# Optimization experiments

Hardware: AMD Instinct MI355X
Metric: run time of the kernel (lower is better)

The kernel has to match this reference:

```python
import jax, jax.numpy as jnp
import numpy as np
from jax import lax

C = 128
HEADS = 8
WS = 8
HIDDEN = C * 4


def _ln2d(x, w, b, eps=1e-6):
    # channel-first LayerNorm over dim 1 of [B,C,H,W]
    u = x.mean(axis=1, keepdims=True)
    s = ((x - u) ** 2).mean(axis=1, keepdims=True)
    xh = (x - u) / jnp.sqrt(s + eps)
    return w[None, :, None, None] * xh + b[None, :, None, None]


def _partition(x, ws):
    # [B,C,H,W] -> [B*nW, ws*ws, C]
    B, C_, H, W = x.shape
    x = x.transpose(0, 2, 3, 1)  # BHWC
    x = x.reshape(B, H // ws, ws, W // ws, ws, C_)
    x = x.transpose(0, 1, 3, 2, 4, 5)
    return x.reshape(-1, ws * ws, C_)


def _reverse(x, ws, H, W, B):
    # [B*nW, ws*ws, C] -> [B,C,H,W]
    C_ = x.shape[-1]
    x = x.reshape(B, H // ws, W // ws, ws, ws, C_)
    x = x.transpose(0, 1, 3, 2, 4, 5).reshape(B, H, W, C_)
    return x.transpose(0, 3, 1, 2)


def setup_inputs() -> dict:
    key = jax.random.key(0)
    ks = jax.random.split(key, 16)
    B, H, W = 4, 256, 256
    inp = {
        "x": jax.random.normal(ks[0], (B, C, H, W), jnp.float32),
        "l0": jax.random.uniform(ks[1], (B, 1, H, W), jnp.float32),
        "norm1_w": jnp.ones((C,), jnp.float32),
        "norm1_b": jnp.zeros((C,), jnp.float32),
        "norm2_w": jnp.ones((C,), jnp.float32),
        "norm2_b": jnp.zeros((C,), jnp.float32),
        "qkv_w": jax.random.normal(ks[2], (3 * C, C), jnp.float32) * (1.0 / np.sqrt(C)),
        "gate_w": jax.random.normal(ks[3], (C,), jnp.float32),
        "gate_b": jnp.zeros((C,), jnp.float32),
        "proj_w": jax.random.normal(ks[4], (C, C), jnp.float32) * (1.0 / np.sqrt(C)),
        "proj_b": jnp.zeros((C,), jnp.float32),
        "ffn_w1": jax.random.normal(ks[5], (HIDDEN, C), jnp.float32) * (1.0 / np.sqrt(C)),
        "ffn_b1": jnp.zeros((HIDDEN,), jnp.float32),
        "ffn_dw": jax.random.normal(ks[6], (HIDDEN, 1, 3, 3), jnp.float32) * (1.0 / 3.0),
        "ffn_dwb": jnp.zeros((HIDDEN,), jnp.float32),
        "ffn_w2": jax.random.normal(ks[7], (C, HIDDEN), jnp.float32) * (1.0 / np.sqrt(HIDDEN)),
        "ffn_b2": jnp.zeros((C,), jnp.float32),
    }
    return inp


def reference(x, l0, norm1_w, norm1_b, norm2_w, norm2_b, qkv_w, gate_w, gate_b,
              proj_w, proj_b, ffn_w1, ffn_b1, ffn_dw, ffn_dwb, ffn_w2, ffn_b2):
    B, C_, H, W = x.shape
    ws = WS
    # H,W chosen divisible by ws -> no padding branch
    head_dim = C_ // HEADS
    scale = head_dim ** -0.5

    shortcut = x
    xn = _ln2d(x, norm1_w, norm1_b)
    qkv = jnp.einsum("oc,bchw->bohw", qkv_w, xn)
    q, k, v = jnp.split(qkv, 3, axis=1)

    # illumination gate (l0 already at [H,W]; bilinear resize to same size is identity)
    gate = jax.nn.sigmoid(l0 * gate_w[None, :, None, None] + gate_b[None, :, None, None])
    q = q * gate

    q = _partition(q, ws)  # [Bw, ws*ws, C]
    k = _partition(k, ws)
    v = _partition(v, ws)
    Bw, N, _ = q.shape
    q = q.reshape(Bw, N, HEADS, head_dim)
    k = k.reshape(Bw, N, HEADS, head_dim)
    v = v.reshape(Bw, N, HEADS, head_dim)

    attn = jnp.einsum("bqhd,bkhd->bhqk", q, k) * scale
    attn = jax.nn.softmax(attn, axis=-1)
    out = jnp.einsum("bhqk,bkhd->bqhd", attn, v).reshape(Bw, N, C_)
    out = _reverse(out, ws, H, W, B)

    out = jnp.einsum("oc,bchw->bohw", proj_w, out) + proj_b[None, :, None, None]
    out = out + shortcut

    # FFN: 1x1 -> GELU -> depthwise 3x3 -> GELU -> 1x1
    h = _ln2d(out, norm2_w, norm2_b)
    h = jnp.einsum("oc,bchw->bohw", ffn_w1, h) + ffn_b1[None, :, None, None]
    h = jax.nn.gelu(h, approximate=False)
    h = lax.conv_general_dilated(h, ffn_dw, window_strides=(1, 1), padding="SAME",
                                 dimension_numbers=("NCHW", "OIHW", "NCHW"),
                                 feature_group_count=HIDDEN)
    h = h + ffn_dwb[None, :, None, None]
    h = jax.nn.gelu(h, approximate=False)
    h = jnp.einsum("oc,bchw->bohw", ffn_w2, h) + ffn_b2[None, :, None, None]
    return out + h
```

## Files before the change

### kernel.cpp

```cpp
#include <hip/hip_runtime.h>
#include <hip/hip_bf16.h>

#define HW   65536
#define CHW  (128*65536)
#define QKV_OZ  33554432u
#define QKV_H   1048576u
#define QKV_WIN 1024u

typedef __attribute__((ext_vector_type(8))) short bf16x8;
typedef __attribute__((ext_vector_type(4))) short bf16x4;
typedef __attribute__((ext_vector_type(4))) float f32x4;

__device__ __forceinline__ float geluf(float v){
    float u = 0.7978845608028654f * v * (1.f + 0.044715f*v*v);
    float e = __expf(2.f*u);
    float th = 1.f - 2.f/(e+1.f);
    return 0.5f*v*(1.f+th);
}

__device__ __forceinline__ float sigmoidf_(float z){
    return 1.f / (1.f + __expf(-z));
}

__device__ __forceinline__ float bf2f(short s){
    return __uint_as_float(((unsigned)(unsigned short)s) << 16);
}

__global__ __launch_bounds__(256) void k_cvt(
    const float* __restrict__ src, __hip_bfloat16* __restrict__ dst, int n)
{
    int i = blockIdx.x*256 + threadIdx.x;
    if (i < n) dst[i] = __float2bfloat16(src[i]);
}

__global__ __launch_bounds__(512,2) void k_ln_qkv_mfma(
    const float* __restrict__ x, const float* __restrict__ l0,
    const float* __restrict__ n1w, const float* __restrict__ n1b,
    const __hip_bfloat16* __restrict__ qkvw, const float* __restrict__ gate_w,
    const float* __restrict__ gate_b, __hip_bfloat16* __restrict__ qkvb)
{
    __shared__ short sxb[128*130];
    __shared__ float sp1[512], sp2[512];
    const int t = threadIdx.x;
    const int lane = t & 63, w = t >> 6;
    const int l15 = lane & 15, q4 = (lane >> 4)*4, ko = (lane >> 4)*8;
    const int mq = w & 3, phalf = w >> 2;
    const int pbase = blockIdx.x * 128;
    const int b = pbase >> 16;
    const int hw0 = pbase & 65535;
    const int x0 = hw0 & 255;
    const int y  = hw0 >> 8;
    const int wy = y >> 3, ty = y & 7;
    const int pxs = t & 127, cq = t >> 7;
    const float* xb = x + (size_t)b*CHW + (size_t)cq*32*HW + hw0 + pxs;
    unsigned* srow = (unsigned*)sxb + pxs*65 + cq*16;

    float s1 = 0.f, s2 = 0.f;
    #pragma unroll
    for (int j = 0; j < 16; ++j) {
        float v0 = xb[(size_t)(2*j)*HW];
        float v1 = xb[(size_t)(2*j+1)*HW];
        s1 += v0 + v1; s2 += v0*v0 + v1*v1;
        __hip_bfloat162 pk = __float22bfloat162_rn(make_float2(v0, v1));
        srow[j] = *(unsigned*)&pk;
    }
    sp1[pxs*4 + cq] = s1;
    sp2[pxs*4 + cq] = s2;
    __syncthreads();
    const float s1t = sp1[pxs*4] + sp1[pxs*4+1] + sp1[pxs*4+2] + sp1[pxs*4+3];
    const float s2t = sp2[pxs*4] + sp2[pxs*4+1] + sp2[pxs*4+2] + sp2[pxs*4+3];
    const float mean = s1t * 0.0078125f;
    const float rstd = rsqrtf(s2t*0.0078125f - mean*mean + 1e-6f);
    #pragma unroll
    for (int j = 0; j < 16; ++j) {
        unsigned u = srow[j];
        float v0 = __uint_as_float(u << 16);
        float v1 = __uint_as_float(u & 0xffff0000u);
        const int c = cq*32 + 2*j;
        v0 = (v0 - mean)*rstd*n1w[c]   + n1b[c];
        v1 = (v1 - mean)*rstd*n1w[c+1] + n1b[c+1];
        __hip_bfloat162 pk = __float22bfloat162_rn(make_float2(v0, v1));
        srow[j] = *(unsigned*)&pk;
    }
    __syncthreads();

    float lv[4];
    #pragma unroll
    for (int nt = 0; nt < 4; ++nt)
        lv[nt] = l0[(size_t)b*HW + hw0 + phalf*64 + nt*16 + l15];

    unsigned toff[4];
    #pragma unroll
    for (int nt = 0; nt < 4; ++nt) {
        const int xg = x0 + phalf*64 + nt*16 + l15;
        toff[nt] = (unsigned)((wy*32 + (xg >> 3))*1024 + (ty*8 + (xg & 7))*16);
    }

    const short* wq = (const short*)qkvw;
    for (int oz = 0; oz < 3; ++oz) {
        f32x4 acc[2][4];
        #pragma unroll
        for (int mt = 0; mt < 2; ++mt)
            #pragma unroll
            for (int nt = 0; nt < 4; ++nt)
                acc[mt][nt] = (f32x4){0.f,0.f,0.f,0.f};
        #pragma unroll
        for (int kc = 0; kc < 4; ++kc) {
            bf16x8 bfrag[4];
            #pragma unroll
            for (int nt = 0; nt < 4; ++nt) {
                const int px = phalf*64 + nt*16 + l15;
                bfrag[nt] = *(const bf16x8*)(sxb + px*130 + kc*32 + ko);
            }
            #pragma unroll
            for (int mt = 0; mt < 2; ++mt) {
                const int m = oz*128 + mq*32 + mt*16 + l15;
                bf16x8 af = *(const bf16x8*)(wq + m*128 + kc*32 + ko);
                #pragma unroll
                for (int nt = 0; nt < 4; ++nt)
                    acc[mt][nt] = __builtin_amdgcn_mfma_f32_16x16x32_bf16(af, bfrag[nt], acc[mt][nt], 0, 0, 0);
            }
        }
        __hip_bfloat16* ob = qkvb + (size_t)oz*QKV_OZ + (size_t)b*8*QKV_H;
        #pragma unroll
        for (int mt = 0; mt < 2; ++mt) {
            const int h = mq*2 + mt;
            #pragma unroll
            for (int nt = 0; nt < 4; ++nt) {
                float v0 = acc[mt][nt][0], v1 = acc[mt][nt][1];
                float v2 = acc[mt][nt][2], v3 = acc[mt][nt][3];
                if (oz == 0) {
                    const int o = h*16 + q4;
                    v0 *= sigmoidf_(lv[nt]*gate_w[o]   + gate_b[o]);
                    v1 *= sigmoidf_(lv[nt]*gate_w[o+1] + gate_b[o+1]);
                    v2 *= sigmoidf_(lv[nt]*gate_w[o+2] + gate_b[o+2]);
                    v3 *= sigmoidf_(lv[nt]*gate_w[o+3] + gate_b[o+3]);
                }
                __hip_bfloat162 p0 = __float22bfloat162_rn(make_float2(v0, v1));
                __hip_bfloat162 p1 = __float22bfloat162_rn(make_float2(v2, v3));
                uint2 st;
                st.x = *(unsigned*)&p0;
                st.y = *(unsigned*)&p1;
                *(uint2*)(ob + (size_t)h*QKV_H + toff[nt] + q4) = st;
            }
        }
    }
}

__global__ __launch_bounds__(256) void k_attn(
    const __hip_bfloat16* __restrict__ qkv, float* __restrict__ attn_out)
{
    __shared__ short vt[4][16*72];
    __shared__ short pt[4][64*68];
    const int t = threadIdx.x;
    const int l = t & 63, w = t >> 6;
    const int c = l & 15, g = l >> 4;
    const int id = blockIdx.x*4 + w;
    const int b = id >> 13;
    const int head = (id >> 10) & 7;
    const int wi = id & 1023;
    const __hip_bfloat16* qp = qkv + ((size_t)(b*8 + head))*QKV_H + (size_t)wi*QKV_WIN;
    const __hip_bfloat16* kp = qp + QKV_OZ;
    const __hip_bfloat16* vp = qp + 2u*QKV_OZ;

    bf16x8 v0 = *(const bf16x8*)(vp + l*16);
    bf16x8 v1 = *(const bf16x8*)(vp + l*16 + 8);
    short* vtw = &vt[w][0];
    #pragma unroll
    for (int d = 0; d < 8; ++d) vtw[d*72 + l] = v0[d];
    #pragma unroll
    for (int d = 0; d < 8; ++d) vtw[(8+d)*72 + l] = v1[d];

    bf16x8 kf[4], qf[4];
    #pragma unroll
    for (int mj = 0; mj < 4; ++mj) {
        if (g < 2) {
            kf[mj] = *(const bf16x8*)(kp + (mj*16 + c)*16 + g*8);
            qf[mj] = *(const bf16x8*)(qp + (mj*16 + c)*16 + g*8);
        } else {
            kf[mj] = (bf16x8){0,0,0,0,0,0,0,0};
            qf[mj] = (bf16x8){0,0,0,0,0,0,0,0};
        }
    }
    f32x4 st[4][4];
    #pragma unroll
    for (int mj = 0; mj < 4; ++mj)
        #pragma unroll
        for (int ni = 0; ni < 4; ++ni)
            st[mj][ni] = (f32x4){0.f,0.f,0.f,0.f};
    #pragma unroll
    for (int mj = 0; mj < 4; ++mj)
        #pragma unroll
        for (int ni = 0; ni < 4; ++ni)
            st[mj][ni] = __builtin_amdgcn_mfma_f32_16x16x32_bf16(kf[mj], qf[ni], st[mj][ni], 0, 0, 0);

    float rs[4];
    bf16x4 pa[4][4], pb[4][4];
    #pragma unroll
    for (int ni = 0; ni < 4; ++ni) {
        float mx = -1e30f;
        #pragma unroll
        for (int mj = 0; mj < 4; ++mj)
            #pragma unroll
            for (int r = 0; r < 4; ++r)
                mx = fmaxf(mx, st[mj][ni][r]);
        mx = fmaxf(mx, __shfl_xor(mx, 16));
        mx = fmaxf(mx, __shfl_xor(mx, 32));
        mx *= 0.25f;
        float sum = 0.f;
        #pragma unroll
        for (int mj = 0; mj < 4; ++mj) {
            float p[4], lo[4];
            #pragma unroll
            for (int r = 0; r < 4; ++r) {
                p[r] = __expf(st[mj][ni][r]*0.25f - mx);
                sum += p[r];
            }
            __hip_bfloat162 h0 = __float22bfloat162_rn(make_float2(p[0], p[1]));
            __hip_bfloat162 h1 = __float22bfloat162_rn(make_float2(p[2], p[3]));
            union { unsigned u[2]; bf16x4 v; } hi;
            hi.u[0] = *(unsigned*)&h0; hi.u[1] = *(unsigned*)&h1;
            pa[mj][ni] = hi.v;
            #pragma unroll
            for (int r = 0; r < 4; ++r) lo[r] = p[r] - bf2f(hi.v[r]);
            __hip_bfloat162 g0 = __float22bfloat162_rn(make_float2(lo[0], lo[1]));
            __hip_bfloat162 g1 = __float22bfloat162_rn(make_float2(lo[2], lo[3]));
            union { unsigned u[2]; bf16x4 v; } lw;
            lw.u[0] = *(unsigned*)&g0; lw.u[1] = *(unsigned*)&g1;
            pb[mj][ni] = lw.v;
        }
        sum += __shfl_xor(sum, 16);
        sum += __shfl_xor(sum, 32);
        rs[ni] = 1.f / sum;
    }

    short* ptw = &pt[w][0];
    f32x4 oc[4];
    #pragma unroll
    for (int ni = 0; ni < 4; ++ni) oc[ni] = (f32x4){0.f,0.f,0.f,0.f};
    bf16x8 vf[2];
    #pragma unroll
    for (int kb = 0; kb < 2; ++kb)
        vf[kb] = *(const bf16x8*)(vtw + c*72 + kb*32 + g*8);

    #pragma unroll
    for (int mj = 0; mj < 4; ++mj)
        #pragma unroll
        for (int ni = 0; ni < 4; ++ni)
            *(bf16x4*)(ptw + (ni*16 + c)*68 + mj*16 + g*4) = pa[mj][ni];
    __syncthreads();
    #pragma unroll
    for (int kb = 0; kb < 2; ++kb)
        #pragma unroll
        for (int ni = 0; ni < 4; ++ni) {
            bf16x8 pf = *(const bf16x8*)(ptw + (ni*16 + c)*68 + kb*32 + g*8);
            oc[ni] = __builtin_amdgcn_mfma_f32_16x16x32_bf16(vf[kb], pf, oc[ni], 0, 0, 0);
        }
    __syncthreads();
    #pragma unroll
    for (int mj = 0; mj < 4; ++mj)
        #pragma unroll
        for (int ni = 0; ni < 4; ++ni)
            *(bf16x4*)(ptw + (ni*16 + c)*68 + mj*16 + g*4) = pb[mj][ni];
    __syncthreads();
    #pragma unroll
    for (int kb = 0; kb < 2; ++kb)
        #pragma unroll
        for (int ni = 0; ni < 4; ++ni) {
            bf16x8 pf = *(const bf16x8*)(ptw + (ni*16 + c)*68 + kb*32 + g*8);
            oc[ni] = __builtin_amdgcn_mfma_f32_16x16x32_bf16(vf[kb], pf, oc[ni], 0, 0, 0);
        }

    const int wy = wi >> 5, wx = wi & 31;
    float* ob = attn_out + (size_t)b*CHW + (size_t)(head*16)*HW + (size_t)(wy*8)*256 + wx*8;
    #pragma unroll
    for (int ni = 0; ni < 4; ++ni) {
        const int tok = ni*16 + c;
        float* o2 = ob + (tok >> 3)*256 + (tok & 7);
        #pragma unroll
        for (int r = 0; r < 4; ++r) {
            const int d = g*4 + r;
            o2[(size_t)d*HW] = oc[ni][r] * rs[ni];
        }
    }
}

__global__ __launch_bounds__(256,3) void k_proj_mfma(
    const float* __restrict__ x, const __hip_bfloat16* __restrict__ projw,
    const float* __restrict__ proj_b, float* __restrict__ out)
{
    __shared__ short sxb[128*130];
    const int t = threadIdx.x;
    const int lane = t & 63, w = t >> 6;
    const int l15 = lane & 15, q4 = (lane >> 4)*4, ko = (lane >> 4)*8;
    const int mhalf = w & 1, phalf = w >> 1;
    const int pbase = blockIdx.x * 128;
    const int b = pbase >> 16;
    const int hw0 = pbase & 65535;
    const int pxs = t & 127, chalf = t >> 7;
    const float* ab = out + (size_t)b*CHW + (size_t)chalf*64*HW + hw0 + pxs;
    unsigned* srow = (unsigned*)sxb + pxs*65 + chalf*32;
    #pragma unroll 8
    for (int j = 0; j < 32; ++j) {
        float v0 = ab[(size_t)(2*j)*HW];
        float v1 = ab[(size_t)(2*j+1)*HW];
        __hip_bfloat162 pk = __float22bfloat162_rn(make_float2(v0, v1));
        srow[j] = *(unsigned*)&pk;
    }
    __syncthreads();
    f32x4 acc[4][4];
    #pragma unroll
    for (int mt = 0; mt < 4; ++mt)
        #pragma unroll
        for (int nt = 0; nt < 4; ++nt)
            acc[mt][nt] = (f32x4){0.f,0.f,0.f,0.f};
    const short* wp = (const short*)projw;
    #pragma unroll
    for (int kc = 0; kc < 4; ++kc) {
        bf16x8 bfrag[4];
        #pragma unroll
        for (int nt = 0; nt < 4; ++nt) {
            const int px = phalf*64 + nt*16 + l15;
            bfrag[nt] = *(const bf16x8*)(sxb + px*130 + kc*32 + ko);
        }
        #pragma unroll
        for (int mt = 0; mt < 4; ++mt) {
            const int m = mhalf*64 + mt*16 + l15;
            bf16x8 af = *(const bf16x8*)(wp + m*128 + kc*32 + ko);
            #pragma unroll
            for (int nt = 0; nt < 4; ++nt)
                acc[mt][nt] = __builtin_amdgcn_mfma_f32_16x16x32_bf16(af, bfrag[nt], acc[mt][nt], 0, 0, 0);
        }
    }
    const float* xb = x + (size_t)b*CHW + hw0;
    float* ob = out + (size_t)b*CHW + hw0;
    #pragma unroll
    for (int mt = 0; mt < 4; ++mt)
        #pragma unroll
        for (int nt = 0; nt < 4; ++nt) {
            const int px = phalf*64 + nt*16 + l15;
            #pragma unroll
            for (int r = 0; r < 4; ++r) {
                const int o = mhalf*64 + mt*16 + q4 + r;
                ob[(size_t)o*HW + px] = acc[mt][nt][r] + proj_b[o] + xb[(size_t)o*HW + px];
            }
        }
}

__global__ __launch_bounds__(256,3) void k_ffn1_mfma(
    const float* __restrict__ outb, const float* __restrict__ n2w, const float* __restrict__ n2b,
    const __hip_bfloat16* __restrict__ w1, const float* __restrict__ b1,
    __hip_bfloat16* __restrict__ h1s)
{
    __shared__ short sxb[128*130];
    __shared__ float sp1[256], sp2[256];
    const int t = threadIdx.x;
    const int lane = t & 63, w = t >> 6;
    const int l15 = lane & 15, q4 = (lane >> 4)*4, ko = (lane >> 4)*8;
    const int mhalf = w & 1, phalf = w >> 1;
    const int hw0 = blockIdx.x * 128;
    const int pxs = t & 127, chalf = t >> 7;
    const float* xb = outb + (size_t)chalf*64*HW + hw0 + pxs;
    unsigned* srow = (unsigned*)sxb + pxs*65 + chalf*32;
    float s1 = 0.f, s2 = 0.f;
    #pragma unroll 8
    for (int j = 0; j < 32; ++j) {
        float v0 = xb[(size_t)(2*j)*HW];
        float v1 = xb[(size_t)(2*j+1)*HW];
        s1 += v0 + v1; s2 += v0*v0 + v1*v1;
        __hip_bfloat162 pk = __float22bfloat162_rn(make_float2(v0, v1));
        srow[j] = *(unsigned*)&pk;
    }
    sp1[pxs*2 + chalf] = s1;
    sp2[pxs*2 + chalf] = s2;
    __syncthreads();
    const float s1t = sp1[pxs*2] + sp1[pxs*2 + 1];
    const float s2t = sp2[pxs*2] + sp2[pxs*2 + 1];
    const float mean = s1t * 0.0078125f;
    const float rstd = rsqrtf(s2t*0.0078125f - mean*mean + 1e-6f);
    #pragma unroll 8
    for (int j = 0; j < 32; ++j) {
        unsigned u = srow[j];
        float v0 = __uint_as_float(u << 16);
        float v1 = __uint_as_float(u & 0xffff0000u);
        const int c = chalf*64 + 2*j;
        v0 = (v0 - mean)*rstd*n2w[c]   + n2b[c];
        v1 = (v1 - mean)*rstd*n2w[c+1] + n2b[c+1];
        __hip_bfloat162 pk = __float22bfloat162_rn(make_float2(v0, v1));
        srow[j] = *(unsigned*)&pk;
    }
    __syncthreads();
    const short* w1s = (const short*)w1;
    __hip_bfloat16* hb = h1s + hw0;
    for (int mc = 0; mc < 4; ++mc) {
        f32x4 acc[4][4];
        #pragma unroll
        for (int mt = 0; mt < 4; ++mt)
            #pragma unroll
            for (int nt = 0; nt < 4; ++nt)
                acc[mt][nt] = (f32x4){0.f,0.f,0.f,0.f};
        #pragma unroll
        for (int kc = 0; kc < 4; ++kc) {
            bf16x8 bfrag[4];
            #pragma unroll
            for (int nt = 0; nt < 4; ++nt) {
                const int px = phalf*64 + nt*16 + l15;
                bfrag[nt] = *(const bf16x8*)(sxb + px*130 + kc*32 + ko);
            }
            #pragma unroll
            for (int mt = 0; mt < 4; ++mt) {
                const int m = mc*128 + mhalf*64 + mt*16 + l15;
                bf16x8 af = *(const bf16x8*)(w1s + m*128 + kc*32 + ko);
                #pragma unroll
                for (int nt = 0; nt < 4; ++nt)
                    acc[mt][nt] = __builtin_amdgcn_mfma_f32_16x16x32_bf16(af, bfrag[nt], acc[mt][nt], 0, 0, 0);
            }
        }
        #pragma unroll
        for (int mt = 0; mt < 4; ++mt)
            #pragma unroll
            for (int nt = 0; nt < 4; ++nt) {
                const int px = phalf*64 + nt*16 + l15;
                #pragma unroll
                for (int r = 0; r < 4; ++r) {
                    const int o = mc*128 + mhalf*64 + mt*16 + q4 + r;
                    const float v = geluf(acc[mt][nt][r] + b1[o]);
                    hb[(size_t)o*HW + px] = __float2bfloat16(v);
                }
            }
    }
}

__global__ __launch_bounds__(256) void k_dwconv(
    const __hip_bfloat16* __restrict__ h1b,
    unsigned* __restrict__ h2u,
    const float* __restrict__ dwf, const float* __restrict__ dwb)
{
    __shared__ short sh[2*18*260];
    const int t = threadIdx.x;
    const int rb = blockIdx.x & 15;
    const int cp = blockIdx.x >> 4;
    const int row0 = rb * 16;
    #pragma unroll
    for (int ch = 0; ch < 2; ++ch) {
        const __hip_bfloat16* src = h1b + (size_t)(cp*2 + ch)*HW;
        #pragma unroll
        for (int i = 0; i < 9; ++i) {
            const int idx = t + i*256;
            const int r = idx >> 7;
            const int u = idx & 127;
            const int y = row0 - 1 + r;
            unsigned v = 0u;
            if ((unsigned)y < 256u) v = *(const unsigned*)(src + (size_t)y*256 + u*2);
            *(unsigned*)(&sh[ch*4680 + r*260 + 2 + u*2]) = v;
        }
    }
    if (t < 72) {
        const int ch = t / 36, q = t - ch*36;
        const int r = q >> 1;
        sh[ch*4680 + r*260 + ((q & 1) ? 258 : 1)] = 0;
    }
    __syncthreads();
    float wt[2][9], bs[2];
    #pragma unroll
    for (int ch = 0; ch < 2; ++ch) {
        const float* dwc = dwf + (size_t)(cp*2 + ch)*9;
        #pragma unroll
        for (int k = 0; k < 9; ++k) wt[ch][k] = dwc[k];
        bs[ch] = dwb[cp*2 + ch];
    }
    const int xp = (t & 127) * 2;
    const int rh = t >> 7;
    #pragma unroll
    for (int r = 0; r < 8; ++r) {
        const int orow = rh*8 + r;
        const int y = row0 + orow;
        float res[2][2];
        #pragma unroll
        for (int ch = 0; ch < 2; ++ch) {
            const short* base = sh + ch*4680 + orow*260 + xp + 1;
            float a[3][4];
            #pragma unroll
            for (int dy = 0; dy < 3; ++dy)
                #pragma unroll
                for (int k = 0; k < 4; ++k)
                    a[dy][k] = __uint_as_float((unsigned)(unsigned short)base[dy*260 + k] << 16);
            #pragma unroll
            for (int xj = 0; xj < 2; ++xj) {
                float s = bs[ch];
                #pragma unroll
                for (int dy = 0; dy < 3; ++dy)
                    #pragma unroll
                    for (int dx = 0; dx < 3; ++dx)
                        s = fmaf(a[dy][xj+dx], wt[ch][dy*3+dx], s);
                res[ch][xj] = geluf(s);
            }
        }
        __hip_bfloat162 pk0 = __float22bfloat162_rn(make_float2(res[0][0], res[1][0]));
        __hip_bfloat162 pk1 = __float22bfloat162_rn(make_float2(res[0][1], res[1][1]));
        uint2 st;
        st.x = *(unsigned*)&pk0;
        st.y = *(unsigned*)&pk1;
        *(uint2*)(h2u + (size_t)cp*HW + (size_t)y*256 + xp) = st;
    }
}

__global__ __launch_bounds__(256,3) void k_ffn2g(
    const unsigned* __restrict__ h2u, const __hip_bfloat16* __restrict__ w2b,
    const float* __restrict__ b2, float* __restrict__ outb)
{
    __shared__ short sxb[128*130];
    const int t = threadIdx.x;
    const int lane = t & 63, w = t >> 6;
    const int l15 = lane & 15, q4 = (lane >> 4)*4, ko = (lane >> 4)*8;
    const int mhalf = w & 1, phalf = w >> 1;
    const int pbase = blockIdx.x * 128;
    const int pxs = t & 127;
    const int chalf = t >> 7;
    f32x4 acc[4][4];
    #pragma unroll
    for (int mt = 0; mt < 4; ++mt)
        #pragma unroll
        for (int nt = 0; nt < 4; ++nt)
            acc[mt][nt] = (f32x4){0.f,0.f,0.f,0.f};
    const short* w2s = (const short*)w2b;
    for (int k4 = 0; k4 < 4; ++k4) {
        if (k4) __syncthreads();
        const unsigned* hsrc = h2u + (size_t)(k4*64 + chalf*32)*HW + pbase + pxs;
        unsigned* sdst = (unsigned*)sxb + pxs*65 + chalf*32;
        #pragma unroll
        for (int c = 0; c < 32; ++c)
            sdst[c] = hsrc[(size_t)c*HW];
        __syncthreads();
        #pragma unroll
        for (int kc = 0; kc < 4; ++kc) {
            bf16x8 bfrag[4];
            #pragma unroll
            for (int nt = 0; nt < 4; ++nt) {
                const int px = phalf*64 + nt*16 + l15;
                bfrag[nt] = *(const bf16x8*)(sxb + px*130 + kc*32 + ko);
            }
            #pragma unroll
            for (int mt = 0; mt < 4; ++mt) {
                const int m = mhalf*64 + mt*16 + l15;
                bf16x8 af = *(const bf16x8*)(w2s + (size_t)m*512 + k4*128 + kc*32 + ko);
                #pragma unroll
                for (int nt = 0; nt < 4; ++nt)
                    acc[mt][nt] = __builtin_amdgcn_mfma_f32_16x16x32_bf16(af, bfrag[nt], acc[mt][nt], 0, 0, 0);
            }
        }
    }
    #pragma unroll
    for (int mt = 0; mt < 4; ++mt)
        #pragma unroll
        for (int nt = 0; nt < 4; ++nt) {
            const int px = pbase + phalf*64 + nt*16 + l15;
            #pragma unroll
            for (int r = 0; r < 4; ++r) {
                const int o = mhalf*64 + mt*16 + q4 + r;
                outb[(size_t)o*HW + px] = acc[mt][nt][r] + b2[o] + outb[(size_t)o*HW + px];
            }
        }
}

extern "C" void kernel_launch(void* const* d_in, const int* in_sizes, int n_in,
                              void* d_out, int out_size, void* d_ws, size_t ws_size,
                              hipStream_t stream) {
    const float* x      = (const float*)d_in[0];
    const float* l0     = (const float*)d_in[1];
    const float* n1w    = (const float*)d_in[2];
    const float* n1b    = (const float*)d_in[3];
    const float* n2w    = (const float*)d_in[4];
    const float* n2b    = (const float*)d_in[5];
    const float* qkv_w  = (const float*)d_in[6];
    const float* gate_w = (const float*)d_in[7];
    const float* gate_b = (const float*)d_in[8];
    const float* proj_w = (const float*)d_in[9];
    const float* proj_b = (const float*)d_in[10];
    const float* ffn_w1 = (const float*)d_in[11];
    const float* ffn_b1 = (const float*)d_in[12];
    const float* ffn_dw = (const float*)d_in[13];
    const float* ffn_dwb= (const float*)d_in[14];
    const float* ffn_w2 = (const float*)d_in[15];
    const float* ffn_b2 = (const float*)d_in[16];

    float* out = (float*)d_out;
    __hip_bfloat16* qkvb = (__hip_bfloat16*)d_ws;
    unsigned* h2u        = (unsigned*)d_ws;
    __hip_bfloat16* h1s  = (__hip_bfloat16*)((char*)d_ws + 201326592);
    char* wbase = (char*)d_ws + 268435456;
    __hip_bfloat16* qkvw_b = (__hip_bfloat16*)(wbase);
    __hip_bfloat16* projw_b= (__hip_bfloat16*)(wbase + 98304);
    __hip_bfloat16* w1b    = (__hip_bfloat16*)(wbase + 131072);
    __hip_bfloat16* w2b    = (__hip_bfloat16*)(wbase + 262144);

    k_cvt<<<dim3(192), dim3(256), 0, stream>>>(qkv_w, qkvw_b, 49152);
    k_cvt<<<dim3(64),  dim3(256), 0, stream>>>(proj_w, projw_b, 16384);
    k_cvt<<<dim3(256), dim3(256), 0, stream>>>(ffn_w1, w1b, 65536);
    k_cvt<<<dim3(256), dim3(256), 0, stream>>>(ffn_w2, w2b, 65536);

    k_ln_qkv_mfma<<<dim3(2048), dim3(512), 0, stream>>>(x, l0, n1w, n1b, qkvw_b, gate_w, gate_b, qkvb);
    k_attn       <<<dim3(8192), dim3(256), 0, stream>>>(qkvb, out);
    k_proj_mfma  <<<dim3(2048), dim3(256), 0, stream>>>(x, projw_b, proj_b, out);
    for (int b = 0; b < 4; ++b) {
        k_ffn1_mfma<<<dim3(512),  dim3(256), 0, stream>>>(out + (size_t)b*CHW, n2w, n2b, w1b, ffn_b1, h1s);
        k_dwconv   <<<dim3(4096), dim3(256), 0, stream>>>(h1s, h2u, ffn_dw, ffn_dwb);
        k_ffn2g    <<<dim3(512),  dim3(256), 0, stream>>>(h2u, w2b, ffn_b2, out + (size_t)b*CHW);
    }
}
```

Before: 1.118 ms.

## Pack attention output as bf16, batch FFN two images per launch, fix LDS reduction layout

```diff
diff --git a/kernel.cpp b/kernel.cpp
--- a/kernel.cpp
+++ b/kernel.cpp
@@ -64,11 +64,11 @@
         __hip_bfloat162 pk = __float22bfloat162_rn(make_float2(v0, v1));
         srow[j] = *(unsigned*)&pk;
     }
-    sp1[pxs*4 + cq] = s1;
-    sp2[pxs*4 + cq] = s2;
-    __syncthreads();
-    const float s1t = sp1[pxs*4] + sp1[pxs*4+1] + sp1[pxs*4+2] + sp1[pxs*4+3];
-    const float s2t = sp2[pxs*4] + sp2[pxs*4+1] + sp2[pxs*4+2] + sp2[pxs*4+3];
+    sp1[cq*128 + pxs] = s1;
+    sp2[cq*128 + pxs] = s2;
+    __syncthreads();
+    const float s1t = sp1[pxs] + sp1[128+pxs] + sp1[256+pxs] + sp1[384+pxs];
+    const float s2t = sp2[pxs] + sp2[128+pxs] + sp2[256+pxs] + sp2[384+pxs];
     const float mean = s1t * 0.0078125f;
     const float rstd = rsqrtf(s2t*0.0078125f - mean*mean + 1e-6f);
     #pragma unroll
@@ -148,7 +148,7 @@
 }
 
 __global__ __launch_bounds__(256) void k_attn(
-    const __hip_bfloat16* __restrict__ qkv, float* __restrict__ attn_out)
+    const __hip_bfloat16* __restrict__ qkv, unsigned* __restrict__ apack)
 {
     __shared__ short vt[4][16*72];
     __shared__ short pt[4][64*68];
@@ -272,21 +272,22 @@
         }
 
     const int wy = wi >> 5, wx = wi & 31;
-    float* ob = attn_out + (size_t)b*CHW + (size_t)(head*16)*HW + (size_t)(wy*8)*256 + wx*8;
+    unsigned* ob = apack + (size_t)b*64*HW + (size_t)(head*8 + g*2)*HW
+                 + (size_t)(wy*8)*256 + wx*8;
     #pragma unroll
     for (int ni = 0; ni < 4; ++ni) {
         const int tok = ni*16 + c;
-        float* o2 = ob + (tok >> 3)*256 + (tok & 7);
-        #pragma unroll
-        for (int r = 0; r < 4; ++r) {
-            const int d = g*4 + r;
-            o2[(size_t)d*HW] = oc[ni][r] * rs[ni];
-        }
+        const int hw = (tok >> 3)*256 + (tok & 7);
+        __hip_bfloat162 p0 = __float22bfloat162_rn(make_float2(oc[ni][0]*rs[ni], oc[ni][1]*rs[ni]));
+        __hip_bfloat162 p1 = __float22bfloat162_rn(make_float2(oc[ni][2]*rs[ni], oc[ni][3]*rs[ni]));
+        ob[hw]            = *(unsigned*)&p0;
+        ob[(size_t)HW+hw] = *(unsigned*)&p1;
     }
 }
 
 __global__ __launch_bounds__(256,3) void k_proj_mfma(
-    const float* __restrict__ x, const __hip_bfloat16* __restrict__ projw,
+    const float* __restrict__ x, const unsigned* __restrict__ apack,
+    const __hip_bfloat16* __restrict__ projw,
     const float* __restrict__ proj_b, float* __restrict__ out)
 {
     __shared__ short sxb[128*130];
@@ -298,15 +299,11 @@
     const int b = pbase >> 16;
     const int hw0 = pbase & 65535;
     const int pxs = t & 127, chalf = t >> 7;
-    const float* ab = out + (size_t)b*CHW + (size_t)chalf*64*HW + hw0 + pxs;
-    unsigned* srow = (unsigned*)sxb + pxs*65 + chalf*32;
-    #pragma unroll 8
-    for (int j = 0; j < 32; ++j) {
-        float v0 = ab[(size_t)(2*j)*HW];
-        float v1 = ab[(size_t)(2*j+1)*HW];
-        __hip_bfloat162 pk = __float22bfloat162_rn(make_float2(v0, v1));
-        srow[j] = *(unsigned*)&pk;
-    }
+    const unsigned* hsrc = apack + (size_t)b*64*HW + (size_t)chalf*32*HW + hw0 + pxs;
+    unsigned* sdst = (unsigned*)sxb + pxs*65 + chalf*32;
+    #pragma unroll
+    for (int c = 0; c < 32; ++c)
+        sdst[c] = hsrc[(size_t)c*HW];
     __syncthreads();
     f32x4 acc[4][4];
     #pragma unroll
@@ -348,7 +345,7 @@
 }
 
 __global__ __launch_bounds__(256,3) void k_ffn1_mfma(
-    const float* __restrict__ outb, const float* __restrict__ n2w, const float* __restrict__ n2b,
+    const float* __restrict__ outb2, const float* __restrict__ n2w, const float* __restrict__ n2b,
     const __hip_bfloat16* __restrict__ w1, const float* __restrict__ b1,
     __hip_bfloat16* __restrict__ h1s)
 {
@@ -358,9 +355,11 @@
     const int lane = t & 63, w = t >> 6;
     const int l15 = lane & 15, q4 = (lane >> 4)*4, ko = (lane >> 4)*8;
     const int mhalf = w & 1, phalf = w >> 1;
-    const int hw0 = blockIdx.x * 128;
+    const int pbase = blockIdx.x * 128;
+    const int b = pbase >> 16;
+    const int hw0 = pbase & 65535;
     const int pxs = t & 127, chalf = t >> 7;
-    const float* xb = outb + (size_t)chalf*64*HW + hw0 + pxs;
+    const float* xb = outb2 + (size_t)b*CHW + (size_t)chalf*64*HW + hw0 + pxs;
     unsigned* srow = (unsigned*)sxb + pxs*65 + chalf*32;
     float s1 = 0.f, s2 = 0.f;
     #pragma unroll 8
@@ -371,11 +370,11 @@
         __hip_bfloat162 pk = __float22bfloat162_rn(make_float2(v0, v1));
         srow[j] = *(unsigned*)&pk;
     }
-    sp1[pxs*2 + chalf] = s1;
-    sp2[pxs*2 + chalf] = s2;
-    __syncthreads();
-    const float s1t = sp1[pxs*2] + sp1[pxs*2 + 1];
-    const float s2t = sp2[pxs*2] + sp2[pxs*2 + 1];
+    sp1[chalf*128 + pxs] = s1;
+    sp2[chalf*128 + pxs] = s2;
+    __syncthreads();
+    const float s1t = sp1[pxs] + sp1[128 + pxs];
+    const float s2t = sp2[pxs] + sp2[128 + pxs];
     const float mean = s1t * 0.0078125f;
     const float rstd = rsqrtf(s2t*0.0078125f - mean*mean + 1e-6f);
     #pragma unroll 8
@@ -391,7 +390,7 @@
     }
     __syncthreads();
     const short* w1s = (const short*)w1;
-    __hip_bfloat16* hb = h1s + hw0;
+    __hip_bfloat16* hb = h1s + (size_t)b*512*HW + hw0;
     for (int mc = 0; mc < 4; ++mc) {
         f32x4 acc[4][4];
         #pragma unroll
@@ -432,15 +431,19 @@
 }
 
 __global__ __launch_bounds__(256) void k_dwconv(
-    const __hip_bfloat16* __restrict__ h1b,
+    const __hip_bfloat16* __restrict__ h1s,
     unsigned* __restrict__ h2u,
     const float* __restrict__ dwf, const float* __restrict__ dwb)
 {
     __shared__ short sh[2*18*260];
     const int t = threadIdx.x;
-    const int rb = blockIdx.x & 15;
-    const int cp = blockIdx.x >> 4;
+    const int blk = blockIdx.x;
+    const int b   = blk >> 12;
+    const int rem = blk & 4095;
+    const int rb = rem & 15;
+    const int cp = rem >> 4;
     const int row0 = rb * 16;
+    const __hip_bfloat16* h1b = h1s + (size_t)b*512*HW;
     #pragma unroll
     for (int ch = 0; ch < 2; ++ch) {
         const __hip_bfloat16* src = h1b + (size_t)(cp*2 + ch)*HW;
@@ -471,6 +474,7 @@
     }
     const int xp = (t & 127) * 2;
     const int rh = t >> 7;
+    unsigned* h2b = h2u + (size_t)b*256*HW;
     #pragma unroll
     for (int r = 0; r < 8; ++r) {
         const int orow = rh*8 + r;
@@ -501,13 +505,13 @@
         uint2 st;
         st.x = *(unsigned*)&pk0;
         st.y = *(unsigned*)&pk1;
-        *(uint2*)(h2u + (size_t)cp*HW + (size_t)y*256 + xp) = st;
+        *(uint2*)(h2b + (size_t)cp*HW + (size_t)y*256 + xp) = st;
     }
 }
 
 __global__ __launch_bounds__(256,3) void k_ffn2g(
     const unsigned* __restrict__ h2u, const __hip_bfloat16* __restrict__ w2b,
-    const float* __restrict__ b2, float* __restrict__ outb)
+    const float* __restrict__ b2, float* __restrict__ outb2)
 {
     __shared__ short sxb[128*130];
     const int t = threadIdx.x;
@@ -515,8 +519,11 @@
     const int l15 = lane & 15, q4 = (lane >> 4)*4, ko = (lane >> 4)*8;
     const int mhalf = w & 1, phalf = w >> 1;
     const int pbase = blockIdx.x * 128;
+    const int b = pbase >> 16;
+    const int hw0 = pbase & 65535;
     const int pxs = t & 127;
     const int chalf = t >> 7;
+    const unsigned* h2b = h2u + (size_t)b*256*HW;
     f32x4 acc[4][4];
     #pragma unroll
     for (int mt = 0; mt < 4; ++mt)
@@ -526,7 +533,7 @@
     const short* w2s = (const short*)w2b;
     for (int k4 = 0; k4 < 4; ++k4) {
         if (k4) __syncthreads();
-        const unsigned* hsrc = h2u + (size_t)(k4*64 + chalf*32)*HW + pbase + pxs;
+        const unsigned* hsrc = h2b + (size_t)(k4*64 + chalf*32)*HW + hw0 + pxs;
         unsigned* sdst = (unsigned*)sxb + pxs*65 + chalf*32;
         #pragma unroll
         for (int c = 0; c < 32; ++c)
@@ -550,15 +557,16 @@
             }
         }
     }
+    float* ob = outb2 + (size_t)b*CHW;
     #pragma unroll
     for (int mt = 0; mt < 4; ++mt)
         #pragma unroll
         for (int nt = 0; nt < 4; ++nt) {
-            const int px = pbase + phalf*64 + nt*16 + l15;
+            const int px = hw0 + phalf*64 + nt*16 + l15;
             #pragma unroll
             for (int r = 0; r < 4; ++r) {
                 const int o = mhalf*64 + mt*16 + q4 + r;
-                outb[(size_t)o*HW + px] = acc[mt][nt][r] + b2[o] + outb[(size_t)o*HW + px];
+                ob[(size_t)o*HW + px] = acc[mt][nt][r] + b2[o] + ob[(size_t)o*HW + px];
             }
         }
 }
@@ -586,8 +594,9 @@
 
     float* out = (float*)d_out;
     __hip_bfloat16* qkvb = (__hip_bfloat16*)d_ws;
-    unsigned* h2u        = (unsigned*)d_ws;
-    __hip_bfloat16* h1s  = (__hip_bfloat16*)((char*)d_ws + 201326592);
+    unsigned* apack      = (unsigned*)((char*)d_ws + 201326592);
+    __hip_bfloat16* h1s  = (__hip_bfloat16*)d_ws;
+    unsigned* h2u        = (unsigned*)((char*)d_ws + 134217728);
     char* wbase = (char*)d_ws + 268435456;
     __hip_bfloat16* qkvw_b = (__hip_bfloat16*)(wbase);
     __hip_bfloat16* projw_b= (__hip_bfloat16*)(wbase + 98304);
@@ -600,11 +609,12 @@
     k_cvt<<<dim3(256), dim3(256), 0, stream>>>(ffn_w2, w2b, 65536);
 
     k_ln_qkv_mfma<<<dim3(2048), dim3(512), 0, stream>>>(x, l0, n1w, n1b, qkvw_b, gate_w, gate_b, qkvb);
-    k_attn       <<<dim3(8192), dim3(256), 0, stream>>>(qkvb, out);
-    k_proj_mfma  <<<dim3(2048), dim3(256), 0, stream>>>(x, projw_b, proj_b, out);
-    for (int b = 0; b < 4; ++b) {
-        k_ffn1_mfma<<<dim3(512),  dim3(256), 0, stream>>>(out + (size_t)b*CHW, n2w, n2b, w1b, ffn_b1, h1s);
-        k_dwconv   <<<dim3(4096), dim3(256), 0, stream>>>(h1s, h2u, ffn_dw, ffn_dwb);
-        k_ffn2g    <<<dim3(512),  dim3(256), 0, stream>>>(h2u, w2b, ffn_b2, out + (size_t)b*CHW);
-    }
-}
+    k_attn       <<<dim3(8192), dim3(256), 0, stream>>>(qkvb, apack);
+    k_proj_mfma  <<<dim3(2048), dim3(256), 0, stream>>>(x, apack, projw_b, proj_b, out);
+    for (int b2 = 0; b2 < 2; ++b2) {
+        float* outp = out + (size_t)b2*2*CHW;
+        k_ffn1_mfma<<<dim3(1024), dim3(256), 0, stream>>>(outp, n2w, n2b, w1b, ffn_b1, h1s);
+        k_dwconv   <<<dim3(8192), dim3(256), 0, stream>>>(h1s, h2u, ffn_dw, ffn_dwb);
+        k_ffn2g    <<<dim3(1024), dim3(256), 0, stream>>>(h2u, w2b, ffn_b2, outp);
+    }
+}
```

New measurement: 1.086 ms. 2.9% less time.
